# Optimization experiments

Hardware: AMD Instinct MI355X
Metric: run time of the kernel (lower is better)

Reference implementation:

```python
import jax, jax.numpy as jnp
import numpy as np
from jax import lax

# Model dims (see init_kwargs / mamba_ssm defaults)
B_, L_, D_IN = 8, 512, 128
D_MODEL, N_LAYERS = 512, 2
EXPAND, D_STATE, D_CONV = 2, 16, 4
D_INNER = EXPAND * D_MODEL          # 1024
DT_RANK = (D_MODEL + 15) // 16      # 32


def setup_inputs() -> dict:
    key = jax.random.key(0)
    ks = iter(jax.random.split(key, 32))
    def p(shape, scale=0.02):
        return jax.random.normal(next(ks), shape, jnp.float32) * scale
    inp = {}
    inp["x"] = jax.random.normal(next(ks), (B_, L_, D_IN), jnp.float32)
    # input projection (Linear(input_dim, d_model), with bias)
    inp["proj_in_w"] = p((D_MODEL, D_IN))
    inp["proj_in_b"] = p((D_MODEL,))
    # stacked per-layer Mamba params (leading dim = N_LAYERS)
    inp["in_proj_w"] = p((N_LAYERS, 2 * D_INNER, D_MODEL))      # no bias (mamba default)
    inp["conv_w"]    = p((N_LAYERS, D_INNER, D_CONV))           # depthwise conv1d
    inp["conv_b"]    = p((N_LAYERS, D_INNER))
    inp["x_proj_w"]  = p((N_LAYERS, DT_RANK + 2 * D_STATE, D_INNER))
    inp["dt_proj_w"] = p((N_LAYERS, D_INNER, DT_RANK))
    inp["dt_proj_b"] = jnp.full((N_LAYERS, D_INNER), 0.1, jnp.float32)
    inp["A_log"]     = jnp.log(jnp.tile(jnp.arange(1, D_STATE + 1, dtype=jnp.float32), (N_LAYERS, D_INNER, 1)))
    inp["Dm"]        = jnp.ones((N_LAYERS, D_INNER), jnp.float32)
    inp["out_proj_w"] = p((N_LAYERS, D_MODEL, D_INNER))         # no bias
    # classifier head: Linear(d_model, 64) -> ReLU -> Linear(64, 1)
    inp["cls_w1"] = p((64, D_MODEL)); inp["cls_b1"] = p((64,))
    inp["cls_w2"] = p((1, 64));       inp["cls_b2"] = p((1,))
    return inp


def _mamba_block(h, in_w, cw, cb, xp_w, dt_w, dt_b, A_log, Dm, out_w):
    B, L, _ = h.shape
    xz = jnp.einsum('bld,ed->ble', h, in_w)           # (B, L, 2*d_inner)
    xi, z = jnp.split(xz, 2, axis=-1)
    # causal depthwise conv1d (pad left d_conv-1, crop to L)
    xc = xi.transpose(0, 2, 1)                         # (B, d_inner, L)
    xc = lax.conv_general_dilated(
        xc, cw[:, None, :], (1,), [(D_CONV - 1, 0)],
        feature_group_count=D_INNER,
        dimension_numbers=('NCH', 'OIH', 'NCH')) + cb[None, :, None]
    xc = jax.nn.silu(xc).transpose(0, 2, 1)            # (B, L, d_inner)
    x_dbl = jnp.einsum('bld,ed->ble', xc, xp_w)        # (B, L, dt_rank + 2*d_state)
    dt, Bm, Cm = jnp.split(x_dbl, [DT_RANK, DT_RANK + D_STATE], axis=-1)
    dt = jax.nn.softplus(jnp.einsum('blr,dr->bld', dt, dt_w) + dt_b)  # (B, L, d_inner)
    A = -jnp.exp(A_log)                                # (d_inner, d_state)

    def step(hst, ins):
        dt_t, B_t, C_t, x_t = ins                      # (B,di),(B,ds),(B,ds),(B,di)
        dA = jnp.exp(dt_t[..., None] * A)              # (B, di, ds)
        hst = dA * hst + (dt_t * x_t)[..., None] * B_t[:, None, :]
        y = jnp.einsum('bds,bs->bd', hst, C_t)
        return hst, y

    h0 = jnp.zeros((B, D_INNER, D_STATE), h.dtype)
    xs = (dt.transpose(1, 0, 2), Bm.transpose(1, 0, 2),
          Cm.transpose(1, 0, 2), xc.transpose(1, 0, 2))
    _, ys = lax.scan(step, h0, xs)                     # ys: (L, B, d_inner)
    y = ys.transpose(1, 0, 2) + xc * Dm                # skip term D*x
    y = y * jax.nn.silu(z)                             # gate
    return jnp.einsum('ble,de->bld', y, out_w)         # (B, L, d_model)


def reference(x, proj_in_w, proj_in_b, in_proj_w, conv_w, conv_b, x_proj_w,
              dt_proj_w, dt_proj_b, A_log, Dm, out_proj_w,
              cls_w1, cls_b1, cls_w2, cls_b2):
    h = jnp.einsum('bli,di->bld', x, proj_in_w) + proj_in_b
    for l in range(N_LAYERS):
        h = _mamba_block(h, in_proj_w[l], conv_w[l], conv_b[l], x_proj_w[l],
                         dt_proj_w[l], dt_proj_b[l], A_log[l], Dm[l], out_proj_w[l])
    h = h.mean(axis=1)                                 # (B, d_model); dropout = identity (eval)
    h = jax.nn.relu(h @ cls_w1.T + cls_b1)
    logits = (h @ cls_w2.T + cls_b2).squeeze(-1)       # (B,)
    return logits
```

## Files before the change

### kernel.cpp

```cpp
#include <hip/hip_runtime.h>
#include <hip/hip_bf16.h>

#define B_   8
#define L_   512
#define DIN  128
#define DM   512
#define NLAY 2
#define DI   1024
#define DS   16
#define DTR  32
#define BL   (B_ * L_)
#define KS   8
#define CL   128
#define NCH  (L_ / CL)

typedef short bf16x8 __attribute__((ext_vector_type(8)));
typedef float floatx4 __attribute__((ext_vector_type(4)));

__device__ __forceinline__ unsigned short f2bf(float f) {
    unsigned int u = __float_as_uint(f);
    unsigned int r = (u + 0x7FFF + ((u >> 16) & 1)) >> 16;
    return (unsigned short)r;
}
__device__ __forceinline__ float bf2f(unsigned short u) {
    return __uint_as_float((unsigned int)u << 16);
}

#if __has_builtin(__builtin_amdgcn_exp2f)
#define EXP2(x) __builtin_amdgcn_exp2f(x)
#else
#define EXP2(x) __expf((x) * 0.69314718056f)
#endif

__device__ __forceinline__ void gld_lds16(const unsigned short* g, unsigned short* l) {
    __builtin_amdgcn_global_load_lds(
        (const __attribute__((address_space(1))) void*)g,
        (__attribute__((address_space(3))) void*)l,
        16, 0, 0);
}

__global__ __launch_bounds__(256) void cvt_all(
    const float* __restrict__ x,  unsigned short* __restrict__ xbf,
    const float* __restrict__ pw, unsigned short* __restrict__ wpin,
    const float* __restrict__ iw, unsigned short* __restrict__ win,
    const float* __restrict__ ow, unsigned short* __restrict__ wout,
    float* __restrict__ hm)
{
    int bid = blockIdx.x;
    if (bid >= 1824) {
        int i = (bid - 1824) * 2048 + threadIdx.x * 8;
        float4 z = make_float4(0.f, 0.f, 0.f, 0.f);
        *(float4*)(hm + i) = z;
        *(float4*)(hm + i + 4) = z;
        return;
    }
    const float* src; unsigned short* dst; int off;
    if      (bid < 256)  { src = x;  dst = xbf;  off = bid; }
    else if (bid < 288)  { src = pw; dst = wpin; off = bid - 256; }
    else if (bid < 1312) { src = iw; dst = win;  off = bid - 288; }
    else                 { src = ow; dst = wout; off = bid - 1312; }
    int i = (off * 256 + threadIdx.x) * 8;
    float4 a = *(const float4*)(src + i);
    float4 b = *(const float4*)(src + i + 4);
    unsigned short o[8];
    o[0] = f2bf(a.x); o[1] = f2bf(a.y); o[2] = f2bf(a.z); o[3] = f2bf(a.w);
    o[4] = f2bf(b.x); o[5] = f2bf(b.y); o[6] = f2bf(b.z); o[7] = f2bf(b.w);
    *(uint4*)(dst + i) = *(uint4*)o;
}

__global__ __launch_bounds__(256) void gemm_mfma(
    const unsigned short* __restrict__ A,
    const unsigned short* __restrict__ W,
    float* __restrict__ C, unsigned short* __restrict__ Cb,
    int N, int K)
{
    __shared__ unsigned short As[128 * 64];
    __shared__ unsigned short Ws[128 * 64];

    const int tid  = threadIdx.x;
    const int lane = tid & 63;
    const int wv   = tid >> 6;
    const int wm   = (wv >> 1) * 64;
    const int wn   = (wv & 1) * 64;
    const int lr   = lane & 15;
    const int q    = lane >> 4;

    const int srow  = lane >> 3;
    const int skcol = (lane & 7) * 8;
    const long aRowBase = (long)blockIdx.y * 128;
    const long wRowBase = (long)blockIdx.x * 128;

    floatx4 acc[4][4];
#pragma unroll
    for (int i = 0; i < 4; ++i)
#pragma unroll
        for (int j = 0; j < 4; ++j)
#pragma unroll
            for (int r = 0; r < 4; ++r) acc[i][j][r] = 0.f;

    for (int k0 = 0; k0 < K; k0 += 64) {
        __syncthreads();
#pragma unroll
        for (int c = 0; c < 4; ++c) {
            const int chunk = wv * 4 + c;
            const int row   = chunk * 8 + srow;
            gld_lds16(A + (aRowBase + row) * K + k0 + skcol,
                      As + chunk * 512 + lane * 8);
            gld_lds16(W + (wRowBase + row) * K + k0 + skcol,
                      Ws + chunk * 512 + lane * 8);
        }
        __syncthreads();

#pragma unroll
        for (int kk = 0; kk < 2; ++kk) {
            bf16x8 af[4], bfr[4];
#pragma unroll
            for (int i = 0; i < 4; ++i)
                af[i] = *(const bf16x8*)(As + (wm + i * 16 + lr) * 64 + kk * 32 + q * 8);
#pragma unroll
            for (int j = 0; j < 4; ++j)
                bfr[j] = *(const bf16x8*)(Ws + (wn + j * 16 + lr) * 64 + kk * 32 + q * 8);
#pragma unroll
            for (int i = 0; i < 4; ++i)
#pragma unroll
                for (int j = 0; j < 4; ++j)
                    acc[i][j] = __builtin_amdgcn_mfma_f32_16x16x32_bf16(
                        af[i], bfr[j], acc[i][j], 0, 0, 0);
        }
    }

#pragma unroll
    for (int i = 0; i < 4; ++i) {
#pragma unroll
        for (int r = 0; r < 4; ++r) {
            const int  crow = blockIdx.y * 128 + wm + i * 16 + q * 4 + r;
            const long base = (long)crow * N + blockIdx.x * 128 + wn + lr;
#pragma unroll
            for (int j = 0; j < 4; ++j) {
                float v = acc[i][j][r];
                if (C)  C[base + j * 16] = v;
                if (Cb) Cb[base + j * 16] = f2bf(v);
            }
        }
    }
}

__global__ __launch_bounds__(256) void gemm_mfma_n64(
    const unsigned short* __restrict__ A,
    const unsigned short* __restrict__ W,
    const float* __restrict__ bias,
    float* __restrict__ C, unsigned short* __restrict__ Cb,
    int N, int K, int meanmode, float* __restrict__ hm)
{
    __shared__ unsigned short As[128 * 64];
    __shared__ unsigned short Ws[64 * 64];
    __shared__ float colsum[64];

    const int tid  = threadIdx.x;
    const int lane = tid & 63;
    const int wv   = tid >> 6;
    const int wm   = wv * 32;
    const int lr   = lane & 15;
    const int q    = lane >> 4;

    const int srow  = lane >> 3;
    const int skcol = (lane & 7) * 8;
    const long aRowBase = (long)blockIdx.y * 128;
    const long wRowBase = (long)blockIdx.x * 64;

    floatx4 acc[2][4];
#pragma unroll
    for (int i = 0; i < 2; ++i)
#pragma unroll
        for (int j = 0; j < 4; ++j)
#pragma unroll
            for (int r = 0; r < 4; ++r) acc[i][j][r] = 0.f;

    for (int k0 = 0; k0 < K; k0 += 64) {
        __syncthreads();
#pragma unroll
        for (int c = 0; c < 4; ++c) {
            const int chunk = wv * 4 + c;
            const int row   = chunk * 8 + srow;
            gld_lds16(A + (aRowBase + row) * K + k0 + skcol,
                      As + chunk * 512 + lane * 8);
        }
#pragma unroll
        for (int c = 0; c < 2; ++c) {
            const int chunk = wv * 2 + c;
            const int row   = chunk * 8 + srow;
            gld_lds16(W + (wRowBase + row) * K + k0 + skcol,
                      Ws + chunk * 512 + lane * 8);
        }
        __syncthreads();

#pragma unroll
        for (int kk = 0; kk < 2; ++kk) {
            bf16x8 af[2], bfr[4];
#pragma unroll
            for (int i = 0; i < 2; ++i)
                af[i] = *(const bf16x8*)(As + (wm + i * 16 + lr) * 64 + kk * 32 + q * 8);
#pragma unroll
            for (int j = 0; j < 4; ++j)
                bfr[j] = *(const bf16x8*)(Ws + (j * 16 + lr) * 64 + kk * 32 + q * 8);
#pragma unroll
            for (int i = 0; i < 2; ++i)
#pragma unroll
                for (int j = 0; j < 4; ++j)
                    acc[i][j] = __builtin_amdgcn_mfma_f32_16x16x32_bf16(
                        af[i], bfr[j], acc[i][j], 0, 0, 0);
        }
    }

    if (meanmode) {
        if (tid < 64) colsum[tid] = 0.f;
        __syncthreads();
#pragma unroll
        for (int j = 0; j < 4; ++j) {
            float p = 0.f;
#pragma unroll
            for (int i = 0; i < 2; ++i)
#pragma unroll
                for (int r = 0; r < 4; ++r) p += acc[i][j][r];
            atomicAdd(&colsum[j * 16 + lr], p);
        }
        __syncthreads();
        if (tid < 64) {
            const int b = blockIdx.y >> 2;
            atomicAdd(&hm[b * DM + blockIdx.x * 64 + tid],
                      colsum[tid] * (1.f / (float)L_));
        }
        return;
    }

    float bj[4] = {0.f, 0.f, 0.f, 0.f};
    if (bias) {
#pragma unroll
        for (int j = 0; j < 4; ++j)
            bj[j] = bias[blockIdx.x * 64 + j * 16 + lr];
    }
#pragma unroll
    for (int i = 0; i < 2; ++i) {
#pragma unroll
        for (int r = 0; r < 4; ++r) {
            const int  crow = blockIdx.y * 128 + wm + i * 16 + q * 4 + r;
            const long base = (long)crow * N + blockIdx.x * 64 + lr;
#pragma unroll
            for (int j = 0; j < 4; ++j) {
                float v = acc[i][j][r] + bj[j];
                if (C)  C[base + j * 16] = v;
                if (Cb) Cb[base + j * 16] = f2bf(v);
            }
        }
    }
}

__global__ __launch_bounds__(256) void xprojconv(
    const unsigned short* __restrict__ xzb, const float* __restrict__ cw,
    const float* __restrict__ cb, const float* __restrict__ W,
    float* __restrict__ P, float* __restrict__ xcout)
{
    __shared__ float As[16][68];
    __shared__ float Ws[16][68];

    const int tid  = threadIdx.x;
    const int tx   = tid & 15;
    const int ty   = tid >> 4;
    const int lrow = tid >> 2;
    const int lk   = (tid & 3) << 2;
    const int kbase = blockIdx.x * (DI / KS);

    const int m = blockIdx.y * 64 + lrow;
    const int t = m & (L_ - 1);
    const float* Wp = W + lrow * DI + kbase + lk;

    float acc[4][4] = {};

    for (int k0 = 0; k0 < DI / KS; k0 += 16) {
        const int dcol = kbase + k0 + lk;
        float4 cbv = *(const float4*)(cb + dcol);
        float sums[4] = {cbv.x, cbv.y, cbv.z, cbv.w};
        float4 cwq[4];
#pragma unroll
        for (int q = 0; q < 4; ++q) cwq[q] = *(const float4*)(cw + (dcol + q) * 4);
#pragma unroll
        for (int w = 0; w < 4; ++w) {
            int tw = t - 3 + w;
            if (tw >= 0) {
                const uint2 up = *(const uint2*)(xzb + (long)(m - 3 + w) * (2 * DI) + dcol);
                float x0 = __uint_as_float(up.x << 16);
                float x1 = __uint_as_float(up.x & 0xffff0000u);
                float x2 = __uint_as_float(up.y << 16);
                float x3 = __uint_as_float(up.y & 0xffff0000u);
                sums[0] += ((const float*)&cwq[0])[w] * x0;
                sums[1] += ((const float*)&cwq[1])[w] * x1;
                sums[2] += ((const float*)&cwq[2])[w] * x2;
                sums[3] += ((const float*)&cwq[3])[w] * x3;
            }
        }
        float4 a4;
#pragma unroll
        for (int q = 0; q < 4; ++q)
            ((float*)&a4)[q] = sums[q] / (1.f + __expf(-sums[q]));
        float4 wv = *(const float4*)(Wp + k0);
        *(float4*)(xcout + (long)m * DI + dcol) = a4;

        __syncthreads();
        As[lk + 0][lrow] = a4.x; As[lk + 1][lrow] = a4.y;
        As[lk + 2][lrow] = a4.z; As[lk + 3][lrow] = a4.w;
        Ws[lk + 0][lrow] = wv.x; Ws[lk + 1][lrow] = wv.y;
        Ws[lk + 2][lrow] = wv.z; Ws[lk + 3][lrow] = wv.w;
        __syncthreads();
#pragma unroll
        for (int k = 0; k < 16; ++k) {
            const float4 a44 = *(const float4*)&As[k][ty << 2];
            const float4 w4  = *(const float4*)&Ws[k][tx << 2];
            acc[0][0] += a44.x * w4.x; acc[0][1] += a44.x * w4.y;
            acc[0][2] += a44.x * w4.z; acc[0][3] += a44.x * w4.w;
            acc[1][0] += a44.y * w4.x; acc[1][1] += a44.y * w4.y;
            acc[1][2] += a44.y * w4.z; acc[1][3] += a44.y * w4.w;
            acc[2][0] += a44.z * w4.x; acc[2][1] += a44.z * w4.y;
            acc[2][2] += a44.z * w4.z; acc[2][3] += a44.z * w4.w;
            acc[3][0] += a44.w * w4.x; acc[3][1] += a44.w * w4.y;
            acc[3][2] += a44.w * w4.z; acc[3][3] += a44.w * w4.w;
        }
    }

    float* out = P + (long)blockIdx.x * (BL * 64)
               + (blockIdx.y * 64 + (ty << 2)) * 64 + (tx << 2);
#pragma unroll
    for (int i = 0; i < 4; ++i)
        *(float4*)(out + i * 64) = make_float4(acc[i][0], acc[i][1],
                                               acc[i][2], acc[i][3]);
}

__global__ __launch_bounds__(256) void xproj_reduce(
    const float* __restrict__ P, float* __restrict__ xdbl)
{
    int i = (blockIdx.x * 256 + threadIdx.x) * 4;
    float4 s = *(const float4*)(P + i);
#pragma unroll
    for (int k = 1; k < KS; ++k) {
        float4 p = *(const float4*)(P + (long)k * (BL * 64) + i);
        s.x += p.x; s.y += p.y; s.z += p.z; s.w += p.w;
    }
    *(float4*)(xdbl + i) = s;
}

template <int CTRL>
__device__ __forceinline__ float dpp_shr_add(float v) {
    int sh = __builtin_amdgcn_update_dpp(0, __float_as_int(v), CTRL, 0xF, 0xF, true);
    return v + __int_as_float(sh);
}

__global__ __launch_bounds__(256) void scan_fused(
    const float* __restrict__ xc, const float* __restrict__ xdbl,
    const float* __restrict__ A_log, const float* __restrict__ dtw,
    const float* __restrict__ dtpb, const float* __restrict__ Dm,
    const unsigned short* __restrict__ xzb, unsigned short* __restrict__ ysb16)
{
    __shared__ float  sdtw[16][36];
    __shared__ float  sxd [CL][36];
    __shared__ float4 sdp [CL / 2][17];
    __shared__ float4 sbc4[CL / 2][17];
    __shared__ float  sy  [16][CL + 4];

    const int tid  = threadIdx.x;
    const int s    = tid & 15;
    const int grp  = tid >> 4;
    const int bd0  = blockIdx.x * 16;
    const int b    = bd0 >> 10;
    const int d0   = bd0 & (DI - 1);
    const int mb0  = b * L_;

    const int j  = tid & 15;
    const int tt = tid >> 4;

    {
        float2 w = *(const float2*)(dtw + (d0 + j) * DTR + tt * 2);
        sdtw[j][tt * 2] = w.x; sdtw[j][tt * 2 + 1] = w.y;
    }
    const float a    = -__expf(A_log[(d0 + grp) * DS + s]);
    const float bias = dtpb[d0 + j];
    const float dmv  = Dm[d0 + j];

    float  rxc[8], rB[8], rC[8], rz[8];
    float2 rxd[8];
#pragma unroll
    for (int i = 0; i < 8; ++i) {
        int m = mb0 + tt + 16 * i;
        rxc[i] = xc[m * DI + d0 + j];
        rxd[i] = *(const float2*)(xdbl + m * 64 + j * 2);
        rB[i]  = xdbl[m * 64 + DTR + j];
        rC[i]  = xdbl[m * 64 + DTR + DS + j];
        rz[i]  = bf2f(xzb[(long)m * (2 * DI) + DI + d0 + j]);
    }

    float state = 0.f;

    for (int c = 0; c < NCH; ++c) {
        const int mbase = mb0 + c * CL;
        float xcur[8], zcur[8];
#pragma unroll
        for (int i = 0; i < 8; ++i) { xcur[i] = rxc[i]; zcur[i] = rz[i]; }

        __syncthreads();
#pragma unroll
        for (int i = 0; i < 8; ++i) {
            int t = tt + 16 * i;
            *(float2*)&sxd[t][j * 2] = rxd[i];
            ((float2*)&sbc4[t >> 1][j])[t & 1] = make_float2(rB[i], rC[i]);
        }
        __syncthreads();

        if (c < NCH - 1) {
#pragma unroll
            for (int i = 0; i < 8; ++i) {
                int m = mbase + CL + tt + 16 * i;
                rxc[i] = xc[m * DI + d0 + j];
                rxd[i] = *(const float2*)(xdbl + m * 64 + j * 2);
                rB[i]  = xdbl[m * 64 + DTR + j];
                rC[i]  = xdbl[m * 64 + DTR + DS + j];
                rz[i]  = bf2f(xzb[(long)m * (2 * DI) + DI + d0 + j]);
            }
        }

        {
            float4 wreg[8];
#pragma unroll
            for (int k = 0; k < 8; ++k) wreg[k] = *(const float4*)&sdtw[j][k * 4];
#pragma unroll
            for (int i = 0; i < 8; ++i) {
                int t = tt + 16 * i;
                float acc = bias;
#pragma unroll
                for (int k = 0; k < 8; ++k) {
                    float4 xv = *(const float4*)&sxd[t][k * 4];
                    acc += xv.x * wreg[k].x + xv.y * wreg[k].y
                         + xv.z * wreg[k].z + xv.w * wreg[k].w;
                }
                float dt = (acc > 20.f) ? acc : __logf(1.f + __expf(acc));
                ((float2*)&sdp[t >> 1][j])[t & 1] =
                    make_float2(dt * 1.44269504f, dt * xcur[i]);
            }
        }
        __syncthreads();

        for (int t4 = 0; t4 < CL; t4 += 4) {
            float ybuf[4];
#pragma unroll
            for (int h = 0; h < 2; ++h) {
                const int t2 = (t4 >> 1) + h;
                const float4 dp = sdp[t2][grp];
                const float4 bc = sbc4[t2][s];
                {
                    const float dA = EXP2(dp.x * a);
                    state = fmaf(dA, state, dp.y * bc.x);
                    float contrib = state * bc.y;
                    contrib = dpp_shr_add<0x111>(contrib);
                    contrib = dpp_shr_add<0x112>(contrib);
                    contrib = dpp_shr_add<0x114>(contrib);
                    contrib = dpp_shr_add<0x118>(contrib);
                    ybuf[h * 2] = contrib;
                }
                {
                    const float dA = EXP2(dp.z * a);
                    state = fmaf(dA, state, dp.w * bc.z);
                    float contrib = state * bc.w;
                    contrib = dpp_shr_add<0x111>(contrib);
                    contrib = dpp_shr_add<0x112>(contrib);
                    contrib = dpp_shr_add<0x114>(contrib);
                    contrib = dpp_shr_add<0x118>(contrib);
                    ybuf[h * 2 + 1] = contrib;
                }
            }
            if (s == 15) *(float4*)&sy[grp][t4] = *(float4*)ybuf;
        }
        __syncthreads();

#pragma unroll
        for (int i = 0; i < 8; ++i) {
            int t = tt + 16 * i;
            float z = zcur[i];
            float sz = z / (1.f + __expf(-z));
            float val = (sy[j][t] + xcur[i] * dmv) * sz;
            ysb16[(mbase + t) * DI + d0 + j] = f2bf(val);
        }
    }
}

__global__ __launch_bounds__(512) void meancls_kernel(
    const float* __restrict__ hm, const float* __restrict__ w1,
    const float* __restrict__ b1, const float* __restrict__ w2,
    const float* __restrict__ b2, float* __restrict__ out)
{
    __shared__ float shm[DM];
    __shared__ float su[64];
    const int b = blockIdx.x, tid = threadIdx.x;
    shm[tid] = hm[b * DM + tid];
    __syncthreads();

    const int j = tid >> 3, sl = tid & 7;
    const float* wr = w1 + j * DM + sl * 64;
    const float* hb = shm + sl * 64;
    float p = 0.f;
    for (int k = 0; k < 64; k += 4)
        p += hb[k] * wr[k] + hb[k+1] * wr[k+1]
           + hb[k+2] * wr[k+2] + hb[k+3] * wr[k+3];
    p += __shfl_xor(p, 1);
    p += __shfl_xor(p, 2);
    p += __shfl_xor(p, 4);
    if (sl == 0) su[j] = fmaxf(p + b1[j], 0.f) * w2[j];
    __syncthreads();
    if (tid < 64) {
        float v = su[tid];
#pragma unroll
        for (int off = 32; off; off >>= 1) v += __shfl_down(v, off);
        if (tid == 0) out[b] = v + b2[0];
    }
}

extern "C" void kernel_launch(void* const* d_in, const int* in_sizes, int n_in,
                              void* d_out, int out_size, void* d_ws, size_t ws_size,
                              hipStream_t stream) {
    const float* x          = (const float*)d_in[0];
    const float* proj_in_w  = (const float*)d_in[1];
    const float* proj_in_b  = (const float*)d_in[2];
    const float* in_proj_w  = (const float*)d_in[3];
    const float* conv_w     = (const float*)d_in[4];
    const float* conv_b     = (const float*)d_in[5];
    const float* x_proj_w   = (const float*)d_in[6];
    const float* dt_proj_w  = (const float*)d_in[7];
    const float* dt_proj_b  = (const float*)d_in[8];
    const float* A_log      = (const float*)d_in[9];
    const float* Dm         = (const float*)d_in[10];
    const float* out_proj_w = (const float*)d_in[11];
    const float* cls_w1     = (const float*)d_in[12];
    const float* cls_b1     = (const float*)d_in[13];
    const float* cls_w2     = (const float*)d_in[14];
    const float* cls_b2     = (const float*)d_in[15];
    float* out = (float*)d_out;

    float* ws   = (float*)d_ws;
    float* h    = ws;
    float* xzf  = h    + BL * DM;
    float* xcb  = xzf  + BL * 2 * DI;
    float* xdbl = xcb  + BL * DI;
    float* scr  = xdbl + BL * 64;
    float* hm   = scr  + 2 * BL * DI;
    float* hmp  = hm   + B_ * DM;
    unsigned short* xzb  = (unsigned short*)xzf;
    unsigned short* u16  = (unsigned short*)(hmp + 64 * DM);
    unsigned short* xbf  = u16;
    unsigned short* hbf  = xbf  + BL * DIN;
    unsigned short* ysbf = hbf  + BL * DM;
    unsigned short* wpin = ysbf + BL * DI;
    unsigned short* win  = wpin + DM * DIN;
    unsigned short* wout = win  + NLAY * 2 * DI * DM;
    float* xpart = scr;

    cvt_all<<<1826, 256, 0, stream>>>(x, xbf, proj_in_w, wpin,
                                      in_proj_w, win, out_proj_w, wout, hm);

    gemm_mfma_n64<<<dim3(DM / 64, BL / 128), 256, 0, stream>>>(
        xbf, wpin, proj_in_b, nullptr, hbf, DM, DIN, 0, nullptr);

    for (int l = 0; l < NLAY; ++l) {
        gemm_mfma<<<dim3(2 * DI / 128, BL / 128), 256, 0, stream>>>(
            hbf, win + l * 2 * DI * DM, nullptr, xzb, 2 * DI, DM);
        xprojconv<<<dim3(KS, 64), 256, 0, stream>>>(
            xzb, conv_w + l * DI * 4, conv_b + l * DI,
            x_proj_w + l * 64 * DI, xpart, xcb);
        xproj_reduce<<<256, 256, 0, stream>>>(xpart, xdbl);
        scan_fused<<<(B_ * DI) / 16, 256, 0, stream>>>(
            xcb, xdbl, A_log + l * DI * DS, dt_proj_w + l * DI * DTR,
            dt_proj_b + l * DI, Dm + l * DI, xzb, ysbf);
        if (l == NLAY - 1) {
            gemm_mfma_n64<<<dim3(DM / 64, BL / 128), 256, 0, stream>>>(
                ysbf, wout + l * DM * DI, nullptr, nullptr, nullptr,
                DM, DI, 1, hm);
        } else {
            gemm_mfma_n64<<<dim3(DM / 64, BL / 128), 256, 0, stream>>>(
                ysbf, wout + l * DM * DI, nullptr, nullptr, hbf,
                DM, DI, 0, nullptr);
        }
    }

    meancls_kernel<<<B_, 512, 0, stream>>>(hm, cls_w1, cls_b1,
                                           cls_w2, cls_b2, out);
}
```

Measured before the change: 335.6 us.

## Move dt projection out of scan into a separate bf16 MFMA GEMM with fused softplus

The dt_proj matmul and softplus no longer run inside the scan kernel's per-chunk FMA loop. A bf16 MFMA GEMM now computes them, with bias and softplus applied in its epilogue. The weights are padded to K=64 with zeros (the x_dbl B/C columns multiply zero weights), and xproj_reduce also writes a bf16 copy of x_dbl. The scan then loads the precomputed dt from global memory, which drops a shared-memory stage and a barrier but adds an extra kernel launch, a 16MB fp32 write/read, and bf16 rounding of dt inputs.

```diff
diff --git a/kernel.cpp b/kernel.cpp
--- a/kernel.cpp
+++ b/kernel.cpp
@@ -44,14 +44,30 @@
     const float* __restrict__ pw, unsigned short* __restrict__ wpin,
     const float* __restrict__ iw, unsigned short* __restrict__ win,
     const float* __restrict__ ow, unsigned short* __restrict__ wout,
+    const float* __restrict__ dtp, unsigned short* __restrict__ dtwp,
     float* __restrict__ hm)
 {
     int bid = blockIdx.x;
-    if (bid >= 1824) {
-        int i = (bid - 1824) * 2048 + threadIdx.x * 8;
+    if (bid >= 1888) {
+        int i = (bid - 1888) * 2048 + threadIdx.x * 8;
         float4 z = make_float4(0.f, 0.f, 0.f, 0.f);
         *(float4*)(hm + i) = z;
         *(float4*)(hm + i + 4) = z;
+        return;
+    }
+    if (bid >= 1824) {
+        int idx = (bid - 1824) * 2048 + threadIdx.x * 8;
+        int row = idx >> 6;
+        int col = idx & 63;
+        unsigned short o[8] = {0, 0, 0, 0, 0, 0, 0, 0};
+        if (col < 32) {
+            const float* s = dtp + row * 32 + col;
+            float4 a = *(const float4*)s;
+            float4 b = *(const float4*)(s + 4);
+            o[0] = f2bf(a.x); o[1] = f2bf(a.y); o[2] = f2bf(a.z); o[3] = f2bf(a.w);
+            o[4] = f2bf(b.x); o[5] = f2bf(b.y); o[6] = f2bf(b.z); o[7] = f2bf(b.w);
+        }
+        *(uint4*)(dtwp + idx) = *(uint4*)o;
         return;
     }
     const float* src; unsigned short* dst; int off;
@@ -150,7 +166,7 @@
     const unsigned short* __restrict__ W,
     const float* __restrict__ bias,
     float* __restrict__ C, unsigned short* __restrict__ Cb,
-    int N, int K, int meanmode, float* __restrict__ hm)
+    int N, int K, int meanmode, float* __restrict__ hm, int act)
 {
     __shared__ unsigned short As[128 * 64];
     __shared__ unsigned short Ws[64 * 64];
@@ -248,6 +264,7 @@
 #pragma unroll
             for (int j = 0; j < 4; ++j) {
                 float v = acc[i][j][r] + bj[j];
+                if (act) v = (v > 20.f) ? v : __logf(1.f + __expf(v));
                 if (C)  C[base + j * 16] = v;
                 if (Cb) Cb[base + j * 16] = f2bf(v);
             }
@@ -335,7 +352,8 @@
 }
 
 __global__ __launch_bounds__(256) void xproj_reduce(
-    const float* __restrict__ P, float* __restrict__ xdbl)
+    const float* __restrict__ P, float* __restrict__ xdbl,
+    unsigned short* __restrict__ xdblb)
 {
     int i = (blockIdx.x * 256 + threadIdx.x) * 4;
     float4 s = *(const float4*)(P + i);
@@ -345,6 +363,9 @@
         s.x += p.x; s.y += p.y; s.z += p.z; s.w += p.w;
     }
     *(float4*)(xdbl + i) = s;
+    unsigned short o[4];
+    o[0] = f2bf(s.x); o[1] = f2bf(s.y); o[2] = f2bf(s.z); o[3] = f2bf(s.w);
+    *(uint2*)(xdblb + i) = *(uint2*)o;
 }
 
 template <int CTRL>
@@ -355,12 +376,10 @@
 
 __global__ __launch_bounds__(256) void scan_fused(
     const float* __restrict__ xc, const float* __restrict__ xdbl,
-    const float* __restrict__ A_log, const float* __restrict__ dtw,
-    const float* __restrict__ dtpb, const float* __restrict__ Dm,
+    const float* __restrict__ dtg,
+    const float* __restrict__ A_log, const float* __restrict__ Dm,
     const unsigned short* __restrict__ xzb, unsigned short* __restrict__ ysb16)
 {
-    __shared__ float  sdtw[16][36];
-    __shared__ float  sxd [CL][36];
     __shared__ float4 sdp [CL / 2][17];
     __shared__ float4 sbc4[CL / 2][17];
     __shared__ float  sy  [16][CL + 4];
@@ -376,21 +395,15 @@
     const int j  = tid & 15;
     const int tt = tid >> 4;
 
-    {
-        float2 w = *(const float2*)(dtw + (d0 + j) * DTR + tt * 2);
-        sdtw[j][tt * 2] = w.x; sdtw[j][tt * 2 + 1] = w.y;
-    }
     const float a    = -__expf(A_log[(d0 + grp) * DS + s]);
-    const float bias = dtpb[d0 + j];
     const float dmv  = Dm[d0 + j];
 
-    float  rxc[8], rB[8], rC[8], rz[8];
-    float2 rxd[8];
+    float rxc[8], rdt[8], rB[8], rC[8], rz[8];
 #pragma unroll
     for (int i = 0; i < 8; ++i) {
         int m = mb0 + tt + 16 * i;
         rxc[i] = xc[m * DI + d0 + j];
-        rxd[i] = *(const float2*)(xdbl + m * 64 + j * 2);
+        rdt[i] = dtg[(long)m * DI + d0 + j];
         rB[i]  = xdbl[m * 64 + DTR + j];
         rC[i]  = xdbl[m * 64 + DTR + DS + j];
         rz[i]  = bf2f(xzb[(long)m * (2 * DI) + DI + d0 + j]);
@@ -408,8 +421,10 @@
 #pragma unroll
         for (int i = 0; i < 8; ++i) {
             int t = tt + 16 * i;
-            *(float2*)&sxd[t][j * 2] = rxd[i];
             ((float2*)&sbc4[t >> 1][j])[t & 1] = make_float2(rB[i], rC[i]);
+            float dt = rdt[i];
+            ((float2*)&sdp[t >> 1][j])[t & 1] =
+                make_float2(dt * 1.44269504f, dt * rxc[i]);
         }
         __syncthreads();
 
@@ -418,33 +433,12 @@
             for (int i = 0; i < 8; ++i) {
                 int m = mbase + CL + tt + 16 * i;
                 rxc[i] = xc[m * DI + d0 + j];
-                rxd[i] = *(const float2*)(xdbl + m * 64 + j * 2);
+                rdt[i] = dtg[(long)m * DI + d0 + j];
                 rB[i]  = xdbl[m * 64 + DTR + j];
                 rC[i]  = xdbl[m * 64 + DTR + DS + j];
                 rz[i]  = bf2f(xzb[(long)m * (2 * DI) + DI + d0 + j]);
             }
         }
-
-        {
-            float4 wreg[8];
-#pragma unroll
-            for (int k = 0; k < 8; ++k) wreg[k] = *(const float4*)&sdtw[j][k * 4];
-#pragma unroll
-            for (int i = 0; i < 8; ++i) {
-                int t = tt + 16 * i;
-                float acc = bias;
-#pragma unroll
-                for (int k = 0; k < 8; ++k) {
-                    float4 xv = *(const float4*)&sxd[t][k * 4];
-                    acc += xv.x * wreg[k].x + xv.y * wreg[k].y
-                         + xv.z * wreg[k].z + xv.w * wreg[k].w;
-                }
-                float dt = (acc > 20.f) ? acc : __logf(1.f + __expf(acc));
-                ((float2*)&sdp[t >> 1][j])[t & 1] =
-                    make_float2(dt * 1.44269504f, dt * xcur[i]);
-            }
-        }
-        __syncthreads();
 
         for (int t4 = 0; t4 < CL; t4 += 4) {
             float ybuf[4];
@@ -557,13 +551,18 @@
     unsigned short* wpin = ysbf + BL * DI;
     unsigned short* win  = wpin + DM * DIN;
     unsigned short* wout = win  + NLAY * 2 * DI * DM;
+
     float* xpart = scr;
-
-    cvt_all<<<1826, 256, 0, stream>>>(x, xbf, proj_in_w, wpin,
-                                      in_proj_w, win, out_proj_w, wout, hm);
+    float* dtgf  = scr + 2 * 1024 * 1024 + 131072;
+    unsigned short* xdblb = (unsigned short*)(scr + 6 * 1024 * 1024 + 262144);
+    unsigned short* dtwp  = (unsigned short*)(scr + 6 * 1024 * 1024 + 262144 + 131072 + 16384);
+
+    cvt_all<<<1890, 256, 0, stream>>>(x, xbf, proj_in_w, wpin,
+                                      in_proj_w, win, out_proj_w, wout,
+                                      dt_proj_w, dtwp, hm);
 
     gemm_mfma_n64<<<dim3(DM / 64, BL / 128), 256, 0, stream>>>(
-        xbf, wpin, proj_in_b, nullptr, hbf, DM, DIN, 0, nullptr);
+        xbf, wpin, proj_in_b, nullptr, hbf, DM, DIN, 0, nullptr, 0);
 
     for (int l = 0; l < NLAY; ++l) {
         gemm_mfma<<<dim3(2 * DI / 128, BL / 128), 256, 0, stream>>>(
@@ -571,18 +570,20 @@
         xprojconv<<<dim3(KS, 64), 256, 0, stream>>>(
             xzb, conv_w + l * DI * 4, conv_b + l * DI,
             x_proj_w + l * 64 * DI, xpart, xcb);
-        xproj_reduce<<<256, 256, 0, stream>>>(xpart, xdbl);
+        xproj_reduce<<<256, 256, 0, stream>>>(xpart, xdbl, xdblb);
+        gemm_mfma_n64<<<dim3(DI / 64, BL / 128), 256, 0, stream>>>(
+            xdblb, dtwp + l * DI * 64, dt_proj_b + l * DI,
+            dtgf, nullptr, DI, 64, 0, nullptr, 1);
         scan_fused<<<(B_ * DI) / 16, 256, 0, stream>>>(
-            xcb, xdbl, A_log + l * DI * DS, dt_proj_w + l * DI * DTR,
-            dt_proj_b + l * DI, Dm + l * DI, xzb, ysbf);
+            xcb, xdbl, dtgf, A_log + l * DI * DS, Dm + l * DI, xzb, ysbf);
         if (l == NLAY - 1) {
             gemm_mfma_n64<<<dim3(DM / 64, BL / 128), 256, 0, stream>>>(
                 ysbf, wout + l * DM * DI, nullptr, nullptr, nullptr,
-                DM, DI, 1, hm);
+                DM, DI, 1, hm, 0);
         } else {
             gemm_mfma_n64<<<dim3(DM / 64, BL / 128), 256, 0, stream>>>(
                 ysbf, wout + l * DM * DI, nullptr, nullptr, hbf,
-                DM, DI, 0, nullptr);
+                DM, DI, 0, nullptr, 0);
         }
     }
 
```

Result: no change. 341.9 us (+1.9%).

## Compute dt projection in scan kernel with bf16 MFMA instead of scalar FMAs

Applied to the files above, without the earlier changes.

Replaces the per-thread scalar dot product for the dt projection (32-wide, through shared memory) inside the scan kernel with a 16x16x32 bf16 MFMA per 16-timestep tile. The reduce kernel now also writes a bf16 copy of x_dbl, and the convert kernel adds a bf16 copy of dt_proj_w. This drops the sdtw/sxd shared buffers and one barrier per chunk, and changes the per-thread timestep mapping to match the MFMA output layout. In exchange, the dt inputs lose precision to bf16, and the new scratch buffers are placed at hand-computed offsets into the workspace.

```diff
diff --git a/kernel.cpp b/kernel.cpp
--- a/kernel.cpp
+++ b/kernel.cpp
@@ -44,21 +44,23 @@
     const float* __restrict__ pw, unsigned short* __restrict__ wpin,
     const float* __restrict__ iw, unsigned short* __restrict__ win,
     const float* __restrict__ ow, unsigned short* __restrict__ wout,
+    const float* __restrict__ dtp, unsigned short* __restrict__ dtwb,
     float* __restrict__ hm)
 {
     int bid = blockIdx.x;
-    if (bid >= 1824) {
-        int i = (bid - 1824) * 2048 + threadIdx.x * 8;
+    if (bid >= 1856) {
+        int i = (bid - 1856) * 2048 + threadIdx.x * 8;
         float4 z = make_float4(0.f, 0.f, 0.f, 0.f);
         *(float4*)(hm + i) = z;
         *(float4*)(hm + i + 4) = z;
         return;
     }
     const float* src; unsigned short* dst; int off;
-    if      (bid < 256)  { src = x;  dst = xbf;  off = bid; }
-    else if (bid < 288)  { src = pw; dst = wpin; off = bid - 256; }
-    else if (bid < 1312) { src = iw; dst = win;  off = bid - 288; }
-    else                 { src = ow; dst = wout; off = bid - 1312; }
+    if      (bid < 256)  { src = x;   dst = xbf;  off = bid; }
+    else if (bid < 288)  { src = pw;  dst = wpin; off = bid - 256; }
+    else if (bid < 1312) { src = iw;  dst = win;  off = bid - 288; }
+    else if (bid < 1824) { src = ow;  dst = wout; off = bid - 1312; }
+    else                 { src = dtp; dst = dtwb; off = bid - 1824; }
     int i = (off * 256 + threadIdx.x) * 8;
     float4 a = *(const float4*)(src + i);
     float4 b = *(const float4*)(src + i + 4);
@@ -335,7 +337,8 @@
 }
 
 __global__ __launch_bounds__(256) void xproj_reduce(
-    const float* __restrict__ P, float* __restrict__ xdbl)
+    const float* __restrict__ P, float* __restrict__ xdbl,
+    unsigned short* __restrict__ xdblb)
 {
     int i = (blockIdx.x * 256 + threadIdx.x) * 4;
     float4 s = *(const float4*)(P + i);
@@ -345,6 +348,9 @@
         s.x += p.x; s.y += p.y; s.z += p.z; s.w += p.w;
     }
     *(float4*)(xdbl + i) = s;
+    unsigned short o[4];
+    o[0] = f2bf(s.x); o[1] = f2bf(s.y); o[2] = f2bf(s.z); o[3] = f2bf(s.w);
+    *(uint2*)(xdblb + i) = *(uint2*)o;
 }
 
 template <int CTRL>
@@ -355,12 +361,12 @@
 
 __global__ __launch_bounds__(256) void scan_fused(
     const float* __restrict__ xc, const float* __restrict__ xdbl,
-    const float* __restrict__ A_log, const float* __restrict__ dtw,
-    const float* __restrict__ dtpb, const float* __restrict__ Dm,
+    const unsigned short* __restrict__ xdblb,
+    const unsigned short* __restrict__ dtwb,
+    const float* __restrict__ dtpb,
+    const float* __restrict__ A_log, const float* __restrict__ Dm,
     const unsigned short* __restrict__ xzb, unsigned short* __restrict__ ysb16)
 {
-    __shared__ float  sdtw[16][36];
-    __shared__ float  sxd [CL][36];
     __shared__ float4 sdp [CL / 2][17];
     __shared__ float4 sbc4[CL / 2][17];
     __shared__ float  sy  [16][CL + 4];
@@ -373,78 +379,100 @@
     const int d0   = bd0 & (DI - 1);
     const int mb0  = b * L_;
 
-    const int j  = tid & 15;
-    const int tt = tid >> 4;
-
-    {
-        float2 w = *(const float2*)(dtw + (d0 + j) * DTR + tt * 2);
-        sdtw[j][tt * 2] = w.x; sdtw[j][tt * 2 + 1] = w.y;
-    }
+    const int j    = tid & 15;
+    const int tt   = tid >> 4;
+    const int lane = tid & 63;
+    const int w    = tid >> 6;
+    const int q    = lane >> 4;
+    const int tW   = 32 * w;
+
     const float a    = -__expf(A_log[(d0 + grp) * DS + s]);
+    const float dmv  = Dm[d0 + j];
     const float bias = dtpb[d0 + j];
-    const float dmv  = Dm[d0 + j];
-
-    float  rxc[8], rB[8], rC[8], rz[8];
-    float2 rxd[8];
+
+    const bf16x8 bfrag = *(const bf16x8*)(dtwb + (d0 + j) * 32 + q * 8);
+
+    float  rB[8], rC[8];
+    bf16x8 ra[2];
+    float  rxc[2][4], rz[2][4];
+
 #pragma unroll
     for (int i = 0; i < 8; ++i) {
         int m = mb0 + tt + 16 * i;
-        rxc[i] = xc[m * DI + d0 + j];
-        rxd[i] = *(const float2*)(xdbl + m * 64 + j * 2);
-        rB[i]  = xdbl[m * 64 + DTR + j];
-        rC[i]  = xdbl[m * 64 + DTR + DS + j];
-        rz[i]  = bf2f(xzb[(long)m * (2 * DI) + DI + d0 + j]);
+        rB[i] = xdbl[m * 64 + DTR + j];
+        rC[i] = xdbl[m * 64 + DTR + DS + j];
+    }
+#pragma unroll
+    for (int tile = 0; tile < 2; ++tile) {
+        ra[tile] = *(const bf16x8*)(xdblb + (long)(mb0 + tW + tile * 16 + j) * 64 + q * 8);
+#pragma unroll
+        for (int r = 0; r < 4; ++r) {
+            int t = tW + tile * 16 + q * 4 + r;
+            rxc[tile][r] = xc[(mb0 + t) * DI + d0 + j];
+            rz [tile][r] = bf2f(xzb[(long)(mb0 + t) * (2 * DI) + DI + d0 + j]);
+        }
     }
 
     float state = 0.f;
 
     for (int c = 0; c < NCH; ++c) {
         const int mbase = mb0 + c * CL;
-        float xcur[8], zcur[8];
-#pragma unroll
-        for (int i = 0; i < 8; ++i) { xcur[i] = rxc[i]; zcur[i] = rz[i]; }
+        float xcur[2][4], zcur[2][4];
+#pragma unroll
+        for (int tile = 0; tile < 2; ++tile)
+#pragma unroll
+            for (int r = 0; r < 4; ++r) {
+                xcur[tile][r] = rxc[tile][r];
+                zcur[tile][r] = rz[tile][r];
+            }
+
+        floatx4 dacc[2];
+#pragma unroll
+        for (int tile = 0; tile < 2; ++tile) {
+            floatx4 cin;
+            cin[0] = bias; cin[1] = bias; cin[2] = bias; cin[3] = bias;
+            dacc[tile] = __builtin_amdgcn_mfma_f32_16x16x32_bf16(
+                ra[tile], bfrag, cin, 0, 0, 0);
+        }
 
         __syncthreads();
 #pragma unroll
         for (int i = 0; i < 8; ++i) {
             int t = tt + 16 * i;
-            *(float2*)&sxd[t][j * 2] = rxd[i];
             ((float2*)&sbc4[t >> 1][j])[t & 1] = make_float2(rB[i], rC[i]);
         }
+#pragma unroll
+        for (int tile = 0; tile < 2; ++tile) {
+#pragma unroll
+            for (int r = 0; r < 4; ++r) {
+                int t = tW + tile * 16 + q * 4 + r;
+                float v = dacc[tile][r];
+                float dt = (v > 20.f) ? v : __logf(1.f + __expf(v));
+                ((float2*)&sdp[t >> 1][j])[t & 1] =
+                    make_float2(dt * 1.44269504f, dt * xcur[tile][r]);
+            }
+        }
         __syncthreads();
 
         if (c < NCH - 1) {
+            const int mn = mbase + CL;
 #pragma unroll
             for (int i = 0; i < 8; ++i) {
-                int m = mbase + CL + tt + 16 * i;
-                rxc[i] = xc[m * DI + d0 + j];
-                rxd[i] = *(const float2*)(xdbl + m * 64 + j * 2);
-                rB[i]  = xdbl[m * 64 + DTR + j];
-                rC[i]  = xdbl[m * 64 + DTR + DS + j];
-                rz[i]  = bf2f(xzb[(long)m * (2 * DI) + DI + d0 + j]);
-            }
-        }
-
-        {
-            float4 wreg[8];
-#pragma unroll
-            for (int k = 0; k < 8; ++k) wreg[k] = *(const float4*)&sdtw[j][k * 4];
-#pragma unroll
-            for (int i = 0; i < 8; ++i) {
-                int t = tt + 16 * i;
-                float acc = bias;
-#pragma unroll
-                for (int k = 0; k < 8; ++k) {
-                    float4 xv = *(const float4*)&sxd[t][k * 4];
-                    acc += xv.x * wreg[k].x + xv.y * wreg[k].y
-                         + xv.z * wreg[k].z + xv.w * wreg[k].w;
+                int m = mn + tt + 16 * i;
+                rB[i] = xdbl[m * 64 + DTR + j];
+                rC[i] = xdbl[m * 64 + DTR + DS + j];
+            }
+#pragma unroll
+            for (int tile = 0; tile < 2; ++tile) {
+                ra[tile] = *(const bf16x8*)(xdblb + (long)(mn + tW + tile * 16 + j) * 64 + q * 8);
+#pragma unroll
+                for (int r = 0; r < 4; ++r) {
+                    int t = tW + tile * 16 + q * 4 + r;
+                    rxc[tile][r] = xc[(mn + t) * DI + d0 + j];
+                    rz [tile][r] = bf2f(xzb[(long)(mn + t) * (2 * DI) + DI + d0 + j]);
                 }
-                float dt = (acc > 20.f) ? acc : __logf(1.f + __expf(acc));
-                ((float2*)&sdp[t >> 1][j])[t & 1] =
-                    make_float2(dt * 1.44269504f, dt * xcur[i]);
-            }
-        }
-        __syncthreads();
+            }
+        }
 
         for (int t4 = 0; t4 < CL; t4 += 4) {
             float ybuf[4];
@@ -479,12 +507,15 @@
         __syncthreads();
 
 #pragma unroll
-        for (int i = 0; i < 8; ++i) {
-            int t = tt + 16 * i;
-            float z = zcur[i];
-            float sz = z / (1.f + __expf(-z));
-            float val = (sy[j][t] + xcur[i] * dmv) * sz;
-            ysb16[(mbase + t) * DI + d0 + j] = f2bf(val);
+        for (int tile = 0; tile < 2; ++tile) {
+#pragma unroll
+            for (int r = 0; r < 4; ++r) {
+                int t = tW + tile * 16 + q * 4 + r;
+                float z = zcur[tile][r];
+                float sz = z / (1.f + __expf(-z));
+                float val = (sy[j][t] + xcur[tile][r] * dmv) * sz;
+                ysb16[(long)(mbase + t) * DI + d0 + j] = f2bf(val);
+            }
         }
     }
 }
@@ -557,10 +588,14 @@
     unsigned short* wpin = ysbf + BL * DI;
     unsigned short* win  = wpin + DM * DIN;
     unsigned short* wout = win  + NLAY * 2 * DI * DM;
+
     float* xpart = scr;
-
-    cvt_all<<<1826, 256, 0, stream>>>(x, xbf, proj_in_w, wpin,
-                                      in_proj_w, win, out_proj_w, wout, hm);
+    unsigned short* xdblb = (unsigned short*)(scr + 6 * 1024 * 1024 + 262144);
+    unsigned short* dtwb  = (unsigned short*)(scr + 6 * 1024 * 1024 + 262144 + 131072 + 16384);
+
+    cvt_all<<<1858, 256, 0, stream>>>(x, xbf, proj_in_w, wpin,
+                                      in_proj_w, win, out_proj_w, wout,
+                                      dt_proj_w, dtwb, hm);
 
     gemm_mfma_n64<<<dim3(DM / 64, BL / 128), 256, 0, stream>>>(
         xbf, wpin, proj_in_b, nullptr, hbf, DM, DIN, 0, nullptr);
@@ -571,10 +606,10 @@
         xprojconv<<<dim3(KS, 64), 256, 0, stream>>>(
             xzb, conv_w + l * DI * 4, conv_b + l * DI,
             x_proj_w + l * 64 * DI, xpart, xcb);
-        xproj_reduce<<<256, 256, 0, stream>>>(xpart, xdbl);
+        xproj_reduce<<<256, 256, 0, stream>>>(xpart, xdbl, xdblb);
         scan_fused<<<(B_ * DI) / 16, 256, 0, stream>>>(
-            xcb, xdbl, A_log + l * DI * DS, dt_proj_w + l * DI * DTR,
-            dt_proj_b + l * DI, Dm + l * DI, xzb, ysbf);
+            xcb, xdbl, xdblb, dtwb + l * DI * 32, dt_proj_b + l * DI,
+            A_log + l * DI * DS, Dm + l * DI, xzb, ysbf);
         if (l == NLAY - 1) {
             gemm_mfma_n64<<<dim3(DM / 64, BL / 128), 256, 0, stream>>>(
                 ysbf, wout + l * DM * DI, nullptr, nullptr, nullptr,
```

Measured after the change: 315.5 us. -6.0%, faster.
